# Performance work log

Measured on AMD Instinct MI355X. Metric: run time of the kernel, lower is better.

## Reference

```python
import jax, jax.numpy as jnp
import numpy as np

N = 100000          # nodes
E = 1_600_000       # edges (before self-loops)
F_IN = 128          # input node features
H1, C1 = 8, 16      # layer-1 heads / per-head channels (concat -> 128)
NUM_CLASSES = 40
NEG_SLOPE = 0.2


def _gat_conv(x, src, dst, W, a_src, a_dst, b, concat):
    """PyG-style GATConv (eval mode, self-loops already in src/dst)."""
    n = x.shape[0]
    H, C = a_src.shape
    h = (x @ W).reshape(n, H, C)                      # [N,H,C]
    s_src = jnp.einsum('nhc,hc->nh', h, a_src)        # [N,H] per-node src logits
    s_dst = jnp.einsum('nhc,hc->nh', h, a_dst)        # [N,H] per-node dst logits
    e = jax.nn.leaky_relu(s_src[src] + s_dst[dst], NEG_SLOPE)   # [E',H]
    # segment softmax over destination node
    m = jax.ops.segment_max(e, dst, num_segments=n)   # [N,H]
    m = jnp.where(jnp.isfinite(m), m, jnp.zeros_like(m))
    p = jnp.exp(e - m[dst])                           # [E',H]
    denom = jax.ops.segment_sum(p, dst, num_segments=n)
    alpha = p / (denom[dst] + 1e-16)                  # [E',H]
    out = jax.ops.segment_sum(alpha[:, :, None] * h[src], dst, num_segments=n)  # [N,H,C]
    out = out.reshape(n, H * C) if concat else out.mean(axis=1)
    return out + b


def setup_inputs() -> dict:
    key = jax.random.key(0)
    ks = jax.random.split(key, 10)
    glorot = lambda k, shp: jax.random.normal(k, shp, jnp.float32) * np.sqrt(2.0 / (shp[0] + shp[-1] if len(shp) > 1 else shp[0]))
    return {
        'x': jax.random.normal(ks[0], (N, F_IN), jnp.float32),
        'edge_index': jax.random.randint(ks[1], (2, E), 0, N, jnp.int64),
        'W1': glorot(ks[2], (F_IN, H1 * C1)),
        'att_src1': glorot(ks[3], (H1, C1)),
        'att_dst1': glorot(ks[4], (H1, C1)),
        'b1': jnp.zeros((H1 * C1,), jnp.float32),
        'W2': glorot(ks[5], (H1 * C1, NUM_CLASSES)),
        'att_src2': glorot(ks[6], (1, NUM_CLASSES)),
        'att_dst2': glorot(ks[7], (1, NUM_CLASSES)),
        'b2': jnp.zeros((NUM_CLASSES,), jnp.float32),
    }


def reference(x, edge_index, W1, att_src1, att_dst1, b1, W2, att_src2, att_dst2, b2):
    n = x.shape[0]
    loops = jnp.arange(n, dtype=edge_index.dtype)
    src = jnp.concatenate([edge_index[0], loops])     # add self-loops (PyG default)
    dst = jnp.concatenate([edge_index[1], loops])
    h = _gat_conv(x, src, dst, W1, att_src1, att_dst1, b1, concat=True)   # [N,128]
    h = jax.nn.relu(h)
    # dropout: identity in eval mode
    out = _gat_conv(h, src, dst, W2, att_src2, att_dst2, b2, concat=True) # heads=1 -> [N,40]
    return jax.nn.log_softmax(out, axis=1)
```

## Files before the change

kernel.cpp:

```cpp
#include <hip/hip_runtime.h>
#include <math.h>

#define N_NODES 100000
#define F_IN    128
#define H1      8
#define C1      16
#define D1      128
#define NCLS    40
#define NEG     0.2f

typedef unsigned int uint32;
typedef unsigned short ushort16;
typedef float v2f __attribute__((ext_vector_type(2)));

__device__ __forceinline__ ushort16 f2bf(float f) {
    unsigned int u = __float_as_uint(f);
    u += 0x7fffu + ((u >> 16) & 1u);
    return (ushort16)(u >> 16);
}
__device__ __forceinline__ float bf_lo(uint32 p) { return __uint_as_float(p << 16); }
__device__ __forceinline__ float bf_hi(uint32 p) { return __uint_as_float(p & 0xffff0000u); }

#define NG 1563

__global__ __launch_bounds__(256) void gemm1_count_kernel(
    const float* __restrict__ x, const float* __restrict__ W,
    uint32* __restrict__ h8,
    const float* __restrict__ a_src, const float* __restrict__ a_dst,
    float* __restrict__ ssrc, float* __restrict__ sdst,
    const int* __restrict__ ei, int E,
    int* __restrict__ deg, int* __restrict__ rank)
{
    __shared__ float xs[64][132];
    __shared__ float wt[128][68];
    const int bid = blockIdx.x;
    const int tid = threadIdx.x;
    const bool is_gemm = ((bid % 5) == 0) && (bid / 5 < NG);
    if (!is_gemm) {
        int ng_before = bid / 5 + ((bid % 5) ? 1 : 0);
        if (ng_before > NG) ng_before = NG;
        int c = bid - ng_before;
        long long e = (long long)c * 256 + tid;
        if (e < E) rank[e] = atomicAdd(&deg[ei[E + e]], 1);
        return;
    }
    const int row0 = (bid / 5) * 64;
#pragma unroll
    for (int i = 0; i < 8; ++i) {
        int idx = tid + i * 256;
        int r = idx >> 5, c4 = idx & 31;
        float4 v = make_float4(0.f, 0.f, 0.f, 0.f);
        if (row0 + r < N_NODES)
            v = ((const float4*)x)[(size_t)(row0 + r) * 32 + c4];
        *(float4*)&xs[r][c4 * 4] = v;
    }
    const int cg = tid & 15;
    const int rg = tid >> 4;
    float acc[4][8];
#pragma unroll
    for (int i = 0; i < 4; ++i)
#pragma unroll
        for (int j = 0; j < 8; ++j) acc[i][j] = 0.f;

    const int stc = tid & 127;
    const int sth = tid >> 7;
#pragma unroll
    for (int chunk = 0; chunk < 2; ++chunk) {
        const int kbase = chunk * 64;
        __syncthreads();
#pragma unroll
        for (int kk = 0; kk < 8; ++kk) {
            int k = sth * 32 + kk * 4;
            float4 v;
            v.x = W[(size_t)(kbase + k)     * 128 + stc];
            v.y = W[(size_t)(kbase + k + 1) * 128 + stc];
            v.z = W[(size_t)(kbase + k + 2) * 128 + stc];
            v.w = W[(size_t)(kbase + k + 3) * 128 + stc];
            *(float4*)&wt[stc][k] = v;
        }
        __syncthreads();
        for (int k0 = 0; k0 < 64; k0 += 4) {
            float4 wa[8];
#pragma unroll
            for (int j = 0; j < 8; ++j)
                wa[j] = *(const float4*)&wt[cg + 16 * j][k0];
#pragma unroll
            for (int i = 0; i < 4; ++i) {
                float4 hx = *(const float4*)&xs[rg + 16 * i][kbase + k0];
#pragma unroll
                for (int j = 0; j < 8; ++j) {
                    acc[i][j] = fmaf(hx.x, wa[j].x, acc[i][j]);
                    acc[i][j] = fmaf(hx.y, wa[j].y, acc[i][j]);
                    acc[i][j] = fmaf(hx.z, wa[j].z, acc[i][j]);
                    acc[i][j] = fmaf(hx.w, wa[j].w, acc[i][j]);
                }
            }
        }
    }
    __syncthreads();
#pragma unroll
    for (int i = 0; i < 4; ++i)
#pragma unroll
        for (int j = 0; j < 8; ++j)
            xs[rg + 16 * i][cg + 16 * j] = acc[i][j];
    __syncthreads();
#pragma unroll
    for (int t = 0; t < 4; ++t) {
        int task = tid + t * 256;
        int r = task >> 4, g = task & 15;
        if (row0 + r < N_NODES) {
            float4 a = *(const float4*)&xs[r][8 * g];
            float4 b = *(const float4*)&xs[r][8 * g + 4];
            int p0 = __builtin_amdgcn_cvt_pk_fp8_f32(a.x, a.y, 0, false);
            p0     = __builtin_amdgcn_cvt_pk_fp8_f32(a.z, a.w, p0, true);
            int p1 = __builtin_amdgcn_cvt_pk_fp8_f32(b.x, b.y, 0, false);
            p1     = __builtin_amdgcn_cvt_pk_fp8_f32(b.z, b.w, p1, true);
            uint2 pk; pk.x = (uint32)p0; pk.y = (uint32)p1;
            ((uint2*)h8)[(size_t)(row0 + r) * 16 + g] = pk;
        }
    }
#pragma unroll
    for (int t = 0; t < 2; ++t) {
        int task = tid + t * 256;
        int r = task >> 3, hh = task & 7;
        if (row0 + r < N_NODES) {
            float as = 0.f, ad = 0.f;
#pragma unroll
            for (int c = 0; c < 16; ++c) {
                float v = xs[r][hh * 16 + c];
                as = fmaf(v, a_src[hh * 16 + c], as);
                ad = fmaf(v, a_dst[hh * 16 + c], ad);
            }
            ssrc[(row0 + r) * 8 + hh] = as;
            sdst[(row0 + r) * 8 + hh] = ad;
        }
    }
}

__global__ void scan1_kernel(const int* __restrict__ deg,
                             int* __restrict__ incl,
                             int* __restrict__ bsum)
{
    __shared__ int tmp[256];
    int i = blockIdx.x * 256 + threadIdx.x;
    int v = (i < N_NODES) ? deg[i] : 0;
    tmp[threadIdx.x] = v;
    __syncthreads();
    for (int o = 1; o < 256; o <<= 1) {
        int t = (threadIdx.x >= (unsigned)o) ? tmp[threadIdx.x - o] : 0;
        __syncthreads();
        tmp[threadIdx.x] += t;
        __syncthreads();
    }
    if (i < N_NODES) incl[i] = tmp[threadIdx.x];
    if (threadIdx.x == 255) bsum[blockIdx.x] = tmp[255];
}

__global__ void scan2_kernel(int* __restrict__ bsum, int nb)
{
    __shared__ int tmp[512];
    int v = (threadIdx.x < (unsigned)nb) ? bsum[threadIdx.x] : 0;
    tmp[threadIdx.x] = v;
    __syncthreads();
    for (int o = 1; o < 512; o <<= 1) {
        int t = (threadIdx.x >= (unsigned)o) ? tmp[threadIdx.x - o] : 0;
        __syncthreads();
        tmp[threadIdx.x] += t;
        __syncthreads();
    }
    if (threadIdx.x < (unsigned)nb) bsum[threadIdx.x] = tmp[threadIdx.x] - v;
}

__global__ void scan3_kernel(const int* __restrict__ incl,
                             const int* __restrict__ bsum,
                             int* __restrict__ offsets)
{
    int i = blockIdx.x * 256 + threadIdx.x;
    if (i < N_NODES) offsets[i + 1] = incl[i] + bsum[blockIdx.x];
    if (i == 0) offsets[0] = 0;
}

__global__ void scatter_kernel(const int* __restrict__ ei, int E,
                               const int* __restrict__ offsets,
                               const int* __restrict__ rank,
                               int* __restrict__ srcs)
{
    int e = blockIdx.x * blockDim.x + threadIdx.x;
    if (e >= E) return;
    int s = ei[e], d = ei[E + e];
    srcs[offsets[d] + rank[e]] = s;
}

__global__ void gather1_kernel(const uint32* __restrict__ h8,
                               const float* __restrict__ ssrc,
                               const float* __restrict__ sdst,
                               const int* __restrict__ offsets,
                               const int* __restrict__ srcs,
                               const float* __restrict__ b1,
                               float* __restrict__ out)
{
    int d = (blockIdx.x * blockDim.x + threadIdx.x) >> 6;
    int lane = threadIdx.x & 63;
    if (d >= N_NODES) return;
    const int hw = lane & 7;
    const int half = lane >> 5;
    const int u = lane & 31;
    const int hc = u >> 2;
    const float sd_w = sdst[d * H1 + hw];

    float acc0 = 0.f, acc1 = 0.f, acc2 = 0.f, acc3 = 0.f;
    float wsum = 0.f;

    float lgs = ssrc[d * H1 + hc] + sdst[d * H1 + hc];
    lgs = lgs >= 0.f ? lgs : NEG * lgs;
    const float ws_self = __expf(lgs);
    {
        float m = (half == 0) ? ws_self : 0.f;
        uint32 p = h8[(size_t)d * 32 + u];
        v2f lo = __builtin_amdgcn_cvt_pk_f32_fp8((int)p, false);
        v2f hi = __builtin_amdgcn_cvt_pk_f32_fp8((int)p, true);
        acc0 = m * lo[0]; acc1 = m * lo[1];
        acc2 = m * hi[0]; acc3 = m * hi[1];
    }

    const int beg = offsets[d], end = offsets[d + 1];
    int base = beg;
    for (; base + 8 <= end; base += 8) {
        int s_l = srcs[base + (lane >> 3)];
        float lg = ssrc[s_l * H1 + hw] + sd_w;
        lg = lg >= 0.f ? lg : NEG * lg;
        float w_l = __expf(lg);
        wsum += w_l;
#pragma unroll
        for (int t = 0; t < 4; ++t) {
            int j = 2 * t + half;
            int s = __shfl(s_l, j << 3);
            float w = __shfl(w_l, (j << 3) | hc);
            uint32 p = h8[(size_t)s * 32 + u];
            v2f lo = __builtin_amdgcn_cvt_pk_f32_fp8((int)p, false);
            v2f hi = __builtin_amdgcn_cvt_pk_f32_fp8((int)p, true);
            acc0 = fmaf(w, lo[0], acc0);
            acc1 = fmaf(w, lo[1], acc1);
            acc2 = fmaf(w, hi[0], acc2);
            acc3 = fmaf(w, hi[1], acc3);
        }
    }
    int cnt = end - base;
    if (cnt > 0) {
        int s_l = 0; float w_l = 0.f;
        if ((lane >> 3) < cnt) {
            s_l = srcs[base + (lane >> 3)];
            float lg = ssrc[s_l * H1 + hw] + sd_w;
            lg = lg >= 0.f ? lg : NEG * lg;
            w_l = __expf(lg);
        }
        wsum += w_l;
        int steps = (cnt + 1) >> 1;
        for (int t = 0; t < steps; ++t) {
            int j = 2 * t + half;
            int s = __shfl(s_l, j << 3);
            float w = __shfl(w_l, (j << 3) | hc);
            uint32 p = h8[(size_t)s * 32 + u];
            v2f lo = __builtin_amdgcn_cvt_pk_f32_fp8((int)p, false);
            v2f hi = __builtin_amdgcn_cvt_pk_f32_fp8((int)p, true);
            acc0 = fmaf(w, lo[0], acc0);
            acc1 = fmaf(w, lo[1], acc1);
            acc2 = fmaf(w, hi[0], acc2);
            acc3 = fmaf(w, hi[1], acc3);
        }
    }
    wsum += __shfl_xor(wsum, 8);
    wsum += __shfl_xor(wsum, 16);
    wsum += __shfl_xor(wsum, 32);
    float ws = ws_self + __shfl(wsum, hc);
    acc0 += __shfl_xor(acc0, 32);
    acc1 += __shfl_xor(acc1, 32);
    acc2 += __shfl_xor(acc2, 32);
    acc3 += __shfl_xor(acc3, 32);
    if (half == 0) {
        float inv = 1.f / (ws + 1e-16f);
        float4 bb = ((const float4*)b1)[u];
        float4 r;
        r.x = fmaf(acc0, inv, bb.x); r.x = r.x > 0.f ? r.x : 0.f;
        r.y = fmaf(acc1, inv, bb.y); r.y = r.y > 0.f ? r.y : 0.f;
        r.z = fmaf(acc2, inv, bb.z); r.z = r.z > 0.f ? r.z : 0.f;
        r.w = fmaf(acc3, inv, bb.w); r.w = r.w > 0.f ? r.w : 0.f;
        ((float4*)(out + (size_t)d * D1))[u] = r;
    }
}

__global__ __launch_bounds__(256) void gemm2_kernel(
    const float* __restrict__ h, const float* __restrict__ W2,
    ushort16* __restrict__ h2b,
    const float* __restrict__ a_src, const float* __restrict__ a_dst,
    float* __restrict__ ssrc, float* __restrict__ sdst)
{
    __shared__ float w2s[40][132];
    __shared__ float hs[64][132];
    const int row0 = blockIdx.x * 64;
    const int tid = threadIdx.x;
#pragma unroll
    for (int i = 0; i < 20; ++i) {
        int idx = tid + i * 256;
        int k = idx / 40, c = idx % 40;
        w2s[c][k] = W2[idx];
    }
#pragma unroll
    for (int i = 0; i < 8; ++i) {
        int idx = tid + i * 256;
        int r = idx >> 5, c4 = idx & 31;
        float4 v = make_float4(0.f, 0.f, 0.f, 0.f);
        if (row0 + r < N_NODES)
            v = ((const float4*)h)[(size_t)(row0 + r) * 32 + c4];
        *(float4*)&hs[r][c4 * 4] = v;
    }
    __syncthreads();
    const int rr = tid >> 3;
    const int g  = tid & 7;
    float acc[2][5];
#pragma unroll
    for (int t = 0; t < 2; ++t)
#pragma unroll
        for (int j = 0; j < 5; ++j) acc[t][j] = 0.f;
    for (int k0 = 0; k0 < 128; k0 += 4) {
        float4 ha = *(const float4*)&hs[rr][k0];
        float4 hb = *(const float4*)&hs[rr + 32][k0];
#pragma unroll
        for (int j = 0; j < 5; ++j) {
            float4 wv = *(const float4*)&w2s[5 * g + j][k0];
            acc[0][j] = fmaf(ha.x, wv.x, acc[0][j]);
            acc[0][j] = fmaf(ha.y, wv.y, acc[0][j]);
            acc[0][j] = fmaf(ha.z, wv.z, acc[0][j]);
            acc[0][j] = fmaf(ha.w, wv.w, acc[0][j]);
            acc[1][j] = fmaf(hb.x, wv.x, acc[1][j]);
            acc[1][j] = fmaf(hb.y, wv.y, acc[1][j]);
            acc[1][j] = fmaf(hb.z, wv.z, acc[1][j]);
            acc[1][j] = fmaf(hb.w, wv.w, acc[1][j]);
        }
    }
#pragma unroll
    for (int t = 0; t < 2; ++t) {
        int row = row0 + rr + 32 * t;
        if (row < N_NODES) {
#pragma unroll
            for (int j = 0; j < 5; ++j)
                h2b[(size_t)row * 40 + 5 * g + j] = f2bf(acc[t][j]);
        }
    }
    __syncthreads();
#pragma unroll
    for (int t = 0; t < 2; ++t)
#pragma unroll
        for (int j = 0; j < 5; ++j)
            hs[rr + 32 * t][5 * g + j] = acc[t][j];
    __syncthreads();
    if (tid < 64 && row0 + tid < N_NODES) {
        float as = 0.f, ad = 0.f;
#pragma unroll
        for (int c = 0; c < 40; ++c) {
            float v = hs[tid][c];
            as = fmaf(v, a_src[c], as);
            ad = fmaf(v, a_dst[c], ad);
        }
        ssrc[row0 + tid] = as;
        sdst[row0 + tid] = ad;
    }
}

__global__ void gather2_kernel(const uint32* __restrict__ h2b,
                               const float* __restrict__ ssrc,
                               const float* __restrict__ sdst,
                               const int* __restrict__ offsets,
                               const int* __restrict__ srcs,
                               const float* __restrict__ b2,
                               float* __restrict__ out)
{
    int d = (blockIdx.x * blockDim.x + threadIdx.x) >> 6;
    int lane = threadIdx.x & 63;
    if (d >= N_NODES) return;
    const float sd = sdst[d];
    const int g = lane / 20;
    const int c = lane - 20 * g;
    const bool act = lane < (NCLS / 2);
    float acc0 = 0.f, acc1 = 0.f, ws = 0.f;

    {
        float lg = ssrc[d] + sd; lg = lg >= 0.f ? lg : NEG * lg;
        float w = __expf(lg);
        uint32 p = act ? h2b[(size_t)d * 20 + lane] : 0u;
        float m = act ? w : 0.f;
        acc0 = m * bf_lo(p); acc1 = m * bf_hi(p);
        ws = w;
    }
    const int beg = offsets[d], end = offsets[d + 1];
    for (int base = beg; base < end; base += 64) {
        int cnt = end - base; if (cnt > 64) cnt = 64;
        int s_l = 0; float w_l = 0.f;
        if (lane < cnt) {
            s_l = srcs[base + lane];
            float lg = ssrc[s_l] + sd; lg = lg >= 0.f ? lg : NEG * lg;
            w_l = __expf(lg);
        }
        float t = w_l;
#pragma unroll
        for (int o = 32; o > 0; o >>= 1) t += __shfl_xor(t, o);
        ws += t;
        for (int j = 0; j < cnt; j += 3) {
            int jj = j + g;
            int s = __shfl(s_l, jj & 63);
            float w = __shfl(w_l, jj & 63);
            if (g >= 3 || jj >= cnt) w = 0.f;
            uint32 p = h2b[(size_t)s * 20 + c];
            acc0 = fmaf(w, bf_lo(p), acc0);
            acc1 = fmaf(w, bf_hi(p), acc1);
        }
    }
    float r00 = __shfl(acc0, lane + 20), r01 = __shfl(acc0, lane + 40);
    float r10 = __shfl(acc1, lane + 20), r11 = __shfl(acc1, lane + 40);
    float l0 = -INFINITY, l1 = -INFINITY;
    if (act) {
        acc0 += r00 + r01;
        acc1 += r10 + r11;
        float inv = 1.f / (ws + 1e-16f);
        l0 = fmaf(acc0, inv, b2[2 * lane]);
        l1 = fmaf(acc1, inv, b2[2 * lane + 1]);
    }
    float m = fmaxf(l0, l1);
#pragma unroll
    for (int o = 32; o > 0; o >>= 1) m = fmaxf(m, __shfl_xor(m, o));
    float ex = act ? (__expf(l0 - m) + __expf(l1 - m)) : 0.f;
#pragma unroll
    for (int o = 32; o > 0; o >>= 1) ex += __shfl_xor(ex, o);
    float lse = __logf(ex) + m;
    if (act) {
        float2 r; r.x = l0 - lse; r.y = l1 - lse;
        ((float2*)(out + (size_t)d * NCLS))[lane] = r;
    }
}

extern "C" void kernel_launch(void* const* d_in, const int* in_sizes, int n_in,
                              void* d_out, int out_size, void* d_ws, size_t ws_size,
                              hipStream_t stream)
{
    const float* x   = (const float*)d_in[0];
    const int*   ei  = (const int*)  d_in[1];
    const float* W1  = (const float*)d_in[2];
    const float* as1 = (const float*)d_in[3];
    const float* ad1 = (const float*)d_in[4];
    const float* b1  = (const float*)d_in[5];
    const float* W2  = (const float*)d_in[6];
    const float* as2 = (const float*)d_in[7];
    const float* ad2 = (const float*)d_in[8];
    const float* b2  = (const float*)d_in[9];
    float* out = (float*)d_out;
    const int E = in_sizes[1] / 2;

    float* ws = (float*)d_ws;
    size_t off = 0;
    uint32* h1f8 = (uint32*)(ws + off); off += (size_t)N_NODES * 32;
    float* h1r  = ws + off; off += (size_t)N_NODES * D1;
    float* ss1  = ws + off; off += (size_t)N_NODES * H1;
    float* sd1  = ws + off; off += (size_t)N_NODES * H1;
    uint32* h2b = (uint32*)(ws + off); off += (size_t)N_NODES * 20;
    float* ss2  = ws + off; off += N_NODES;
    float* sd2  = ws + off; off += N_NODES;
    int* ib = (int*)(ws + off);
    size_t ioff = 0;
    int* deg     = ib + ioff; ioff += N_NODES;
    int* incl    = ib + ioff; ioff += N_NODES;
    int* offsets = ib + ioff; ioff += N_NODES + 1;
    int* bsum    = ib + ioff; ioff += 512;
    int* rank    = ib + ioff; ioff += E;
    int* srcs    = ib + ioff; ioff += E;

    hipMemsetAsync(deg, 0, (size_t)N_NODES * sizeof(int), stream);

    const int nb = (N_NODES + 255) / 256;
    const int nc = (E + 255) / 256;

    gemm1_count_kernel<<<NG + nc, 256, 0, stream>>>(x, W1, h1f8, as1, ad1,
                                                    ss1, sd1, ei, E, deg, rank);
    scan1_kernel<<<nb, 256, 0, stream>>>(deg, incl, bsum);
    scan2_kernel<<<1, 512, 0, stream>>>(bsum, nb);
    scan3_kernel<<<nb, 256, 0, stream>>>(incl, bsum, offsets);
    scatter_kernel<<<(E + 255) / 256, 256, 0, stream>>>(ei, E, offsets, rank, srcs);

    gather1_kernel<<<(N_NODES * 64 + 255) / 256, 256, 0, stream>>>(h1f8, ss1, sd1, offsets, srcs, b1, h1r);

    gemm2_kernel<<<(N_NODES + 63) / 64, 256, 0, stream>>>(h1r, W2, (ushort16*)h2b, as2, ad2, ss2, sd2);
    gather2_kernel<<<(N_NODES * 64 + 255) / 256, 256, 0, stream>>>(h2b, ss2, sd2, offsets, srcs, b2, out);
}
```

Baseline: 386.7 us.

## Fold edge degree counting into GEMM blocks and drop the separate scan2 kernel

Each GEMM block now also counts the in-degrees for 1024 edges. It issues its atomicAdds on the degree array before the GEMM work and writes the ranks after it, so the atomic latency overlaps the matrix multiply instead of needing separate counting blocks. The scan2 kernel is removed: each scan3 block reduces the preceding block sums itself, which saves one launch at the cost of some redundant reads. This depends on NG*1024 covering all edges, and it adds register pressure to the GEMM blocks.

New measurement: 409.0 us. +5.8%, slower.

```diff
diff --git a/kernel.cpp b/kernel.cpp
--- a/kernel.cpp
+++ b/kernel.cpp
@@ -35,16 +35,19 @@
     __shared__ float wt[128][68];
     const int bid = blockIdx.x;
     const int tid = threadIdx.x;
-    const bool is_gemm = ((bid % 5) == 0) && (bid / 5 < NG);
-    if (!is_gemm) {
-        int ng_before = bid / 5 + ((bid % 5) ? 1 : 0);
-        if (ng_before > NG) ng_before = NG;
-        int c = bid - ng_before;
-        long long e = (long long)c * 256 + tid;
-        if (e < E) rank[e] = atomicAdd(&deg[ei[E + e]], 1);
-        return;
-    }
-    const int row0 = (bid / 5) * 64;
+
+    const long long ebase = (long long)bid * 1024;
+    int dste[4], rnk[4];
+#pragma unroll
+    for (int i = 0; i < 4; ++i) {
+        long long e = ebase + tid + i * 256;
+        dste[i] = (e < E) ? ei[E + e] : -1;
+    }
+#pragma unroll
+    for (int i = 0; i < 4; ++i)
+        rnk[i] = (dste[i] >= 0) ? atomicAdd(&deg[dste[i]], 1) : 0;
+
+    const int row0 = bid * 64;
 #pragma unroll
     for (int i = 0; i < 8; ++i) {
         int idx = tid + i * 256;
@@ -135,6 +138,11 @@
             sdst[(row0 + r) * 8 + hh] = ad;
         }
     }
+#pragma unroll
+    for (int i = 0; i < 4; ++i) {
+        long long e = ebase + tid + i * 256;
+        if (e < E) rank[e] = rnk[i];
+    }
 }
 
 __global__ void scan1_kernel(const int* __restrict__ deg,
@@ -156,27 +164,23 @@
     if (threadIdx.x == 255) bsum[blockIdx.x] = tmp[255];
 }
 
-__global__ void scan2_kernel(int* __restrict__ bsum, int nb)
-{
-    __shared__ int tmp[512];
-    int v = (threadIdx.x < (unsigned)nb) ? bsum[threadIdx.x] : 0;
-    tmp[threadIdx.x] = v;
-    __syncthreads();
-    for (int o = 1; o < 512; o <<= 1) {
-        int t = (threadIdx.x >= (unsigned)o) ? tmp[threadIdx.x - o] : 0;
-        __syncthreads();
-        tmp[threadIdx.x] += t;
-        __syncthreads();
-    }
-    if (threadIdx.x < (unsigned)nb) bsum[threadIdx.x] = tmp[threadIdx.x] - v;
-}
-
 __global__ void scan3_kernel(const int* __restrict__ incl,
                              const int* __restrict__ bsum,
                              int* __restrict__ offsets)
 {
-    int i = blockIdx.x * 256 + threadIdx.x;
-    if (i < N_NODES) offsets[i + 1] = incl[i] + bsum[blockIdx.x];
+    __shared__ int red[256];
+    const int t = threadIdx.x;
+    int s = 0;
+    for (int i = t; i < blockIdx.x; i += 256) s += bsum[i];
+    red[t] = s;
+    __syncthreads();
+    for (int o = 128; o > 0; o >>= 1) {
+        if (t < o) red[t] += red[t + o];
+        __syncthreads();
+    }
+    const int base = red[0];
+    int i = blockIdx.x * 256 + t;
+    if (i < N_NODES) offsets[i + 1] = incl[i] + base;
     if (i == 0) offsets[0] = 0;
 }
 
@@ -476,12 +480,10 @@
     hipMemsetAsync(deg, 0, (size_t)N_NODES * sizeof(int), stream);
 
     const int nb = (N_NODES + 255) / 256;
-    const int nc = (E + 255) / 256;
-
-    gemm1_count_kernel<<<NG + nc, 256, 0, stream>>>(x, W1, h1f8, as1, ad1,
-                                                    ss1, sd1, ei, E, deg, rank);
+
+    gemm1_count_kernel<<<NG, 256, 0, stream>>>(x, W1, h1f8, as1, ad1,
+                                               ss1, sd1, ei, E, deg, rank);
     scan1_kernel<<<nb, 256, 0, stream>>>(deg, incl, bsum);
-    scan2_kernel<<<1, 512, 0, stream>>>(bsum, nb);
     scan3_kernel<<<nb, 256, 0, stream>>>(incl, bsum, offsets);
     scatter_kernel<<<(E + 255) / 256, 256, 0, stream>>>(ei, E, offsets, rank, srcs);
 
```
